# Kernel tuning notes

Measured on AMD Instinct MI355X. Metric: run time of the kernel, lower is better.

The kernel has to match this reference:

```python
import jax, jax.numpy as jnp
import numpy as np

EPS = 1e-5

def batchnorm2d(x, gamma, beta):
    # training-mode BN over (N, T, V) per channel; x: [N, C, T, V]
    mean = jnp.mean(x, axis=(0, 2, 3), keepdims=True)
    var = jnp.var(x, axis=(0, 2, 3), keepdims=True)
    xhat = (x - mean) * jax.lax.rsqrt(var + EPS)
    return xhat * gamma[None, :, None, None] + beta[None, :, None, None]

def temporal_shift(x, theta, stride):
    # learnable per-channel temporal shift with linear interpolation, zero pad
    # x: [N, C, T, V], theta: [C]
    N, C, T, V = x.shape
    T_out = T // stride
    t = jnp.arange(T_out, dtype=theta.dtype)
    pos = t[None, :] * stride + theta[:, None]          # [C, T_out]
    i0 = jnp.floor(pos).astype(jnp.int32)
    frac = (pos - i0.astype(theta.dtype))[None, :, :, None]  # [1,C,T_out,1]
    cidx = jnp.arange(C)[:, None]                        # [C, 1]

    def gather(idx):
        valid = (idx >= 0) & (idx < T)
        g = x[:, cidx, jnp.clip(idx, 0, T - 1), :]       # [N, C, T_out, V]
        return jnp.where(valid[None, :, :, None], g, 0.0)

    return gather(i0) * (1.0 - frac) + gather(i0 + 1) * frac

def setup_inputs() -> dict:
    key = jax.random.key(0)
    k = jax.random.split(key, 6)
    N, Cin, Cout, T, V = 64, 256, 256, 64, 25
    x = jax.random.normal(k[0], (N, Cin, T, V), dtype=jnp.float32)
    # kaiming normal fan_out for 1x1 conv: std = sqrt(2 / (Cout*1*1))
    conv_w = jax.random.normal(k[1], (Cout, Cin), dtype=jnp.float32) * np.float32(np.sqrt(2.0 / Cout))
    conv_b = jnp.zeros((Cout,), dtype=jnp.float32)
    bn1_g = jnp.ones((Cin,), dtype=jnp.float32)
    bn1_b = jnp.zeros((Cin,), dtype=jnp.float32)
    bn2_g = jnp.ones((Cin,), dtype=jnp.float32)   # bn_init(bn2, 1)
    bn2_b = jnp.zeros((Cin,), dtype=jnp.float32)
    theta_in = jax.random.uniform(k[2], (Cin,), jnp.float32, -1.0, 1.0)
    theta_out = jax.random.uniform(k[3], (Cout,), jnp.float32, -1.0, 1.0)
    return {"x": x, "conv_w": conv_w, "conv_b": conv_b,
            "bn1_g": bn1_g, "bn1_b": bn1_b, "bn2_g": bn2_g, "bn2_b": bn2_b,
            "theta_in": theta_in, "theta_out": theta_out}

def reference(x, conv_w, conv_b, bn1_g, bn1_b, bn2_g, bn2_b, theta_in, theta_out):
    stride = 1
    h = batchnorm2d(x, bn1_g, bn1_b)
    h = temporal_shift(h, theta_in, 1)
    h = jnp.einsum('nctv,oc->notv', h, conv_w) + conv_b[None, :, None, None]
    h = jax.nn.relu(h)
    h = temporal_shift(h, theta_out, stride)
    h = batchnorm2d(h, bn2_g, bn2_b)
    return h
```

## Files before the change

### kernel.cpp

```cpp
#include <hip/hip_runtime.h>


#define EPSV 1e-5f
constexpr int Nn = 64, Cc = 256, Tt = 64, Vv = 25;
constexpr int TV = Tt * Vv;
constexpr int CTV = Cc * TV;
constexpr float Minv = 1.0f / (Nn * TV);

typedef short short8 __attribute__((ext_vector_type(8)));
typedef float floatx4 __attribute__((ext_vector_type(4)));

__device__ __forceinline__ unsigned short f2bf(float f) {
    unsigned int u = __builtin_bit_cast(unsigned int, f);
    u += 0x7FFFu + ((u >> 16) & 1u);
    return (unsigned short)(u >> 16);
}
__device__ __forceinline__ float bf2f(unsigned short h) {
    unsigned int u = ((unsigned int)h) << 16;
    return __builtin_bit_cast(float, u);
}
__device__ __forceinline__ void gload_lds16(const void* g, void* l) {
    __builtin_amdgcn_global_load_lds((const __attribute__((address_space(1))) void*)g,
                                     (__attribute__((address_space(3))) void*)l, 16, 0, 0);
}

__global__ __launch_bounds__(256) void k_bn1_stats(const float* __restrict__ x,
                                                   const float* __restrict__ w,
                                                   unsigned short* __restrict__ wb,
                                                   float* __restrict__ sacc,
                                                   float* __restrict__ qacc) {
    int c = blockIdx.y, ng = blockIdx.x, tid = threadIdx.x;
    if (c == 256) {
        int base = ng * 8192 + tid;
#pragma unroll
        for (int i = 0; i < 32; ++i) wb[base + i * 256] = f2bf(w[base + i * 256]);
        return;
    }
    const float* xp = x + (size_t)(ng * 8) * CTV + (size_t)c * TV;
    float s = 0.f, q = 0.f;
    for (int n = 0; n < 8; ++n) {
        const float4* p = (const float4*)(xp + (size_t)n * CTV);
        for (int i = tid; i < 400; i += 256) {
            float4 v = p[i];
            s += (v.x + v.y) + (v.z + v.w);
            q += (v.x * v.x + v.y * v.y) + (v.z * v.z + v.w * v.w);
        }
    }
    for (int off = 32; off; off >>= 1) { s += __shfl_down(s, off); q += __shfl_down(q, off); }
    if ((tid & 63) == 0) { atomicAdd(&sacc[c], s); atomicAdd(&qacc[c], q); }
}

__global__ __launch_bounds__(256) void k_bn1_shift(const float* __restrict__ x,
                                                   const float* __restrict__ sacc,
                                                   const float* __restrict__ qacc,
                                                   const float* __restrict__ g,
                                                   const float* __restrict__ b,
                                                   const float* __restrict__ theta,
                                                   unsigned short* __restrict__ ht) {
    int c0 = blockIdx.x * 16;
    int tile = blockIdx.y;
    int n = blockIdx.z;
    int tid = threadIdx.x;
    __shared__ __attribute__((aligned(16))) float lds[16][460];
    __shared__ float psc[16], ptc[16], pfr[16];
    __shared__ int pdd[16], pww[16];

    if (tid < 16) {
        int c = c0 + tid;
        float mean = sacc[c] * Minv;
        float var = qacc[c] * Minv - mean * mean;
        float sc = g[c] * rsqrtf(var + EPSV);
        float th = theta[c];
        float fd = floorf(th);
        int d = (int)fd;
        pdd[tid] = d;
        pww[tid] = 28 + d * 25;
        pfr[tid] = th - fd;
        psc[tid] = sc;
        ptc[tid] = b[c] - mean * sc;
    }

    int E0 = tile * 400;
    int lo = E0 - 28; if (lo < 0) lo = 0;
    int hi = E0 + 428; if (hi > 1600) hi = 1600;
    int ldsoff = lo - (E0 - 28);
    int nf4 = (hi - lo) >> 2;
    {
        int ci = tid >> 4, li = tid & 15;
        const float4* xrow = (const float4*)(x + (size_t)n * CTV + (size_t)(c0 + ci) * TV + lo);
        float* lrow = &lds[ci][ldsoff];
        for (int i = li; i < nf4; i += 16)
            *(float4*)(lrow + i * 4) = xrow[i];
    }
    __syncthreads();

    int oct = tid & 1, tvr = tid >> 1;
    unsigned short* outb = ht + (size_t)n * CTV + c0 + oct * 8;
    for (int tv_l = tvr; tv_l < 400; tv_l += 128) {
        int e = E0 + tv_l;
        int t = e / 25;
        unsigned int wrds[4];
#pragma unroll
        for (int k = 0; k < 8; ++k) {
            int ci = oct * 8 + k;
            int i0 = t + pdd[ci];
            int w0 = tv_l + pww[ci];
            float x0 = lds[ci][w0];
            float x1 = lds[ci][w0 + 25];
            float sc = psc[ci], tc = ptc[ci], f = pfr[ci];
            float b0 = ((unsigned)i0 < 64u) ? (x0 * sc + tc) : 0.f;
            float b1 = ((unsigned)(i0 + 1) < 64u) ? (x1 * sc + tc) : 0.f;
            unsigned short hb = f2bf(b0 + f * (b1 - b0));
            if (k & 1) wrds[k >> 1] |= ((unsigned int)hb) << 16;
            else       wrds[k >> 1] = hb;
        }
        uint4 st = { wrds[0], wrds[1], wrds[2], wrds[3] };
        *(uint4*)(outb + (size_t)e * 256) = st;
    }
}

__global__ __launch_bounds__(256) void k_gemm(const unsigned short* __restrict__ ht,
                                              const unsigned short* __restrict__ wb,
                                              const float* __restrict__ bias,
                                              unsigned short* __restrict__ y) {
    int j0 = blockIdx.x * 128;
    int o0 = blockIdx.y * 128;
    int tid = threadIdx.x;
    int w = tid >> 6, lane = tid & 63;
    int quad = lane >> 4, l16 = lane & 15;
    __shared__ __attribute__((aligned(16))) unsigned short A[128 * 32];
    __shared__ __attribute__((aligned(16))) unsigned short B[128 * 32];
    floatx4 acc[4][4] = {};
    int srow = w * 32 + (lane >> 2);
    int skcol = (lane & 3) * 8;
    const unsigned short* wp0 = wb + (size_t)(o0 + srow) * 256 + skcol;
    const unsigned short* hp0 = ht + (size_t)(j0 + srow) * 256 + skcol;
    int oh = w >> 1, jh = w & 1;
    for (int k0 = 0; k0 < 256; k0 += 32) {
        __syncthreads();
#pragma unroll
        for (int a = 0; a < 2; ++a) {
            gload_lds16(wp0 + (size_t)a * 16 * 256 + k0, A + (w * 32 + a * 16) * 32);
            gload_lds16(hp0 + (size_t)a * 16 * 256 + k0, B + (w * 32 + a * 16) * 32);
        }
        __syncthreads();
        short8 af[4], bf[4];
#pragma unroll
        for (int m = 0; m < 4; ++m)
            af[m] = *(const short8*)&A[(oh * 64 + m * 16 + l16) * 32 + quad * 8];
#pragma unroll
        for (int jt = 0; jt < 4; ++jt)
            bf[jt] = *(const short8*)&B[(jh * 64 + jt * 16 + l16) * 32 + quad * 8];
#pragma unroll
        for (int m = 0; m < 4; ++m)
#pragma unroll
            for (int jt = 0; jt < 4; ++jt)
                acc[m][jt] = __builtin_amdgcn_mfma_f32_16x16x32_bf16(af[m], bf[jt], acc[m][jt], 0, 0, 0);
    }
    int jbase = j0 + jh * 64;
    int n = jbase / 1600;
    int tvb = jbase - n * 1600;
    unsigned short* yb = y + (size_t)n * CTV + tvb;
#pragma unroll
    for (int m = 0; m < 4; ++m) {
        int o = o0 + oh * 64 + m * 16 + quad * 4;
#pragma unroll
        for (int r = 0; r < 4; ++r) {
            float bia = bias[o + r];
            unsigned short* yrow = yb + (size_t)(o + r) * TV;
#pragma unroll
            for (int jt = 0; jt < 4; ++jt) {
                float vv = acc[m][jt][r] + bia;
                vv = vv > 0.f ? vv : 0.f;
                yrow[jt * 16 + l16] = f2bf(vv);
            }
        }
    }
}

__global__ __launch_bounds__(256) void k_bn2_stats(const unsigned short* __restrict__ y,
                                                   const float* __restrict__ theta,
                                                   float* __restrict__ sacc,
                                                   float* __restrict__ qacc) {
    int o = blockIdx.y, ng = blockIdx.x, tid = threadIdx.x;
    __shared__ __attribute__((aligned(16))) unsigned short row[1600];
    float th = theta[o];
    float fd = floorf(th);
    int d = (int)fd;
    float f = th - fd;
    float s = 0.f, q = 0.f;
    for (int n = ng * 8; n < ng * 8 + 8; ++n) {
        const uint4* yp = (const uint4*)(y + (size_t)n * CTV + (size_t)o * TV);
        __syncthreads();
        if (tid < 200) ((uint4*)row)[tid] = yp[tid];
        __syncthreads();
        for (int e = tid; e < 1600; e += 256) {
            int t = e / 25, v = e - t * 25;
            int i0 = t + d, i1 = i0 + 1;
            float a0 = ((unsigned)i0 < 64u) ? bf2f(row[i0 * 25 + v]) : 0.f;
            float a1 = ((unsigned)i1 < 64u) ? bf2f(row[i1 * 25 + v]) : 0.f;
            float z = (1.f - f) * a0 + f * a1;
            s += z; q += z * z;
        }
    }
    for (int off = 32; off; off >>= 1) { s += __shfl_down(s, off); q += __shfl_down(q, off); }
    if ((tid & 63) == 0) { atomicAdd(&sacc[o], s); atomicAdd(&qacc[o], q); }
}

__global__ __launch_bounds__(256) void k_bn2_apply(const unsigned short* __restrict__ y,
                                                   const float* __restrict__ theta,
                                                   const float* __restrict__ sacc,
                                                   const float* __restrict__ qacc,
                                                   const float* __restrict__ g,
                                                   const float* __restrict__ b,
                                                   float* __restrict__ out) {
    int o = blockIdx.y, n = blockIdx.x, tid = threadIdx.x;
    __shared__ __attribute__((aligned(16))) unsigned short row[1600];
    float th = theta[o];
    float fd = floorf(th);
    int d = (int)fd;
    float f = th - fd;
    float mean = sacc[o] * Minv;
    float var = qacc[o] * Minv - mean * mean;
    float sc = g[o] * rsqrtf(var + EPSV);
    float tc = b[o] - mean * sc;
    const uint4* yp = (const uint4*)(y + (size_t)n * CTV + (size_t)o * TV);
    if (tid < 200) ((uint4*)row)[tid] = yp[tid];
    __syncthreads();
    float4* op = (float4*)(out + (size_t)n * CTV + (size_t)o * TV);
    for (int i = tid; i < 400; i += 256) {
        float4 r;
        int e = i * 4;
#pragma unroll
        for (int k = 0; k < 4; ++k) {
            int ee = e + k;
            int t = ee / 25, v = ee - t * 25;
            int i0 = t + d, i1 = i0 + 1;
            float a0 = ((unsigned)i0 < 64u) ? bf2f(row[i0 * 25 + v]) : 0.f;
            float a1 = ((unsigned)i1 < 64u) ? bf2f(row[i1 * 25 + v]) : 0.f;
            ((float*)&r)[k] = ((1.f - f) * a0 + f * a1) * sc + tc;
        }
        op[i] = r;
    }
}

extern "C" void kernel_launch(void* const* d_in, const int* in_sizes, int n_in,
                              void* d_out, int out_size, void* d_ws, size_t ws_size,
                              hipStream_t stream) {
    const float* x      = (const float*)d_in[0];
    const float* conv_w = (const float*)d_in[1];
    const float* conv_b = (const float*)d_in[2];
    const float* bn1_g  = (const float*)d_in[3];
    const float* bn1_b  = (const float*)d_in[4];
    const float* bn2_g  = (const float*)d_in[5];
    const float* bn2_b  = (const float*)d_in[6];
    const float* th_in  = (const float*)d_in[7];
    const float* th_out = (const float*)d_in[8];
    float* out = (float*)d_out;

    char* ws = (char*)d_ws;
    unsigned short* ht = (unsigned short*)ws;
    unsigned short* yy = (unsigned short*)(ws + 52428800);
    unsigned short* wb = (unsigned short*)(ws + 104857600);
    float* sacc1 = (float*)(ws + 104988672);
    float* qacc1 = sacc1 + 256;
    float* sacc2 = qacc1 + 256;
    float* qacc2 = sacc2 + 256;

    hipMemsetAsync((void*)sacc1, 0, 4 * 256 * sizeof(float), stream);
    hipLaunchKernelGGL(k_bn1_stats, dim3(8, 257), dim3(256), 0, stream,
                       x, conv_w, wb, sacc1, qacc1);
    hipLaunchKernelGGL(k_bn1_shift, dim3(16, 4, 64), dim3(256), 0, stream,
                       x, sacc1, qacc1, bn1_g, bn1_b, th_in, ht);
    hipLaunchKernelGGL(k_gemm, dim3(800, 2), dim3(256), 0, stream, ht, wb, conv_b, yy);
    hipLaunchKernelGGL(k_bn2_stats, dim3(8, 256), dim3(256), 0, stream, yy, th_out, sacc2, qacc2);
    hipLaunchKernelGGL(k_bn2_apply, dim3(64, 256), dim3(256), 0, stream,
                       yy, th_out, sacc2, qacc2, bn2_g, bn2_b, out);
}
```

Baseline: 328.2 us.

## Fold BN1 affine into GEMM weights and fuse BN1 stats with temporal shift

BN1 normalization is folded algebraically into the 1x1 conv: weights are scaled by the per-channel BN scale, and the shift term becomes a per-output bias, with edge corrections at t=0 and t=63 for the zero padding. This lets one kernel read x once, computing BN1 stats and writing the shifted bf16 activations without waiting for stats, which removes a full pass over x. The GEMM tile also grows to cover all 256 outputs per block, and the output is staged through LDS so global stores are coalesced. The risks are bf16 rounding of the raw, unnormalized shifted input and of the scaled weights, the larger LDS and register footprint, and the correctness of the boundary bias corrections.

```diff
diff --git a/kernel.cpp b/kernel.cpp
--- a/kernel.cpp
+++ b/kernel.cpp
@@ -24,157 +24,199 @@
                                      (__attribute__((address_space(3))) void*)l, 16, 0, 0);
 }
 
-__global__ __launch_bounds__(256) void k_bn1_stats(const float* __restrict__ x,
-                                                   const float* __restrict__ w,
-                                                   unsigned short* __restrict__ wb,
-                                                   float* __restrict__ sacc,
-                                                   float* __restrict__ qacc) {
-    int c = blockIdx.y, ng = blockIdx.x, tid = threadIdx.x;
-    if (c == 256) {
-        int base = ng * 8192 + tid;
-#pragma unroll
-        for (int i = 0; i < 32; ++i) wb[base + i * 256] = f2bf(w[base + i * 256]);
-        return;
-    }
-    const float* xp = x + (size_t)(ng * 8) * CTV + (size_t)c * TV;
-    float s = 0.f, q = 0.f;
-    for (int n = 0; n < 8; ++n) {
-        const float4* p = (const float4*)(xp + (size_t)n * CTV);
-        for (int i = tid; i < 400; i += 256) {
-            float4 v = p[i];
-            s += (v.x + v.y) + (v.z + v.w);
-            q += (v.x * v.x + v.y * v.y) + (v.z * v.z + v.w * v.w);
-        }
-    }
-    for (int off = 32; off; off >>= 1) { s += __shfl_down(s, off); q += __shfl_down(q, off); }
-    if ((tid & 63) == 0) { atomicAdd(&sacc[c], s); atomicAdd(&qacc[c], q); }
-}
-
-__global__ __launch_bounds__(256) void k_bn1_shift(const float* __restrict__ x,
-                                                   const float* __restrict__ sacc,
-                                                   const float* __restrict__ qacc,
-                                                   const float* __restrict__ g,
-                                                   const float* __restrict__ b,
-                                                   const float* __restrict__ theta,
-                                                   unsigned short* __restrict__ ht) {
-    int c0 = blockIdx.x * 16;
-    int tile = blockIdx.y;
-    int n = blockIdx.z;
+__global__ __launch_bounds__(256) void k_stats_shift(const float* __restrict__ x,
+                                                     const float* __restrict__ theta,
+                                                     float* __restrict__ sacc,
+                                                     float* __restrict__ qacc,
+                                                     unsigned short* __restrict__ ht) {
+    int c0 = blockIdx.x * 64;
+    int E0 = blockIdx.y * 200;
+    int n  = blockIdx.z;
     int tid = threadIdx.x;
-    __shared__ __attribute__((aligned(16))) float lds[16][460];
-    __shared__ float psc[16], ptc[16], pfr[16];
-    __shared__ int pdd[16], pww[16];
-
-    if (tid < 16) {
-        int c = c0 + tid;
-        float mean = sacc[c] * Minv;
-        float var = qacc[c] * Minv - mean * mean;
-        float sc = g[c] * rsqrtf(var + EPSV);
-        float th = theta[c];
+    __shared__ __attribute__((aligned(16))) float xt[256][68];
+    __shared__ int   pd[64];
+    __shared__ float pf[64];
+    if (tid < 64) {
+        float th = theta[c0 + tid];
         float fd = floorf(th);
-        int d = (int)fd;
-        pdd[tid] = d;
-        pww[tid] = 28 + d * 25;
-        pfr[tid] = th - fd;
-        psc[tid] = sc;
-        ptc[tid] = b[c] - mean * sc;
-    }
-
-    int E0 = tile * 400;
+        pd[tid] = (int)fd;
+        pf[tid] = th - fd;
+    }
     int lo = E0 - 28; if (lo < 0) lo = 0;
-    int hi = E0 + 428; if (hi > 1600) hi = 1600;
+    int hi = E0 + 228; if (hi > 1600) hi = 1600;
     int ldsoff = lo - (E0 - 28);
     int nf4 = (hi - lo) >> 2;
     {
-        int ci = tid >> 4, li = tid & 15;
+        int ci = tid >> 2, li = tid & 3;
         const float4* xrow = (const float4*)(x + (size_t)n * CTV + (size_t)(c0 + ci) * TV + lo);
-        float* lrow = &lds[ci][ldsoff];
-        for (int i = li; i < nf4; i += 16)
-            *(float4*)(lrow + i * 4) = xrow[i];
-    }
-    __syncthreads();
-
-    int oct = tid & 1, tvr = tid >> 1;
-    unsigned short* outb = ht + (size_t)n * CTV + c0 + oct * 8;
-    for (int tv_l = tvr; tv_l < 400; tv_l += 128) {
+        for (int i = li; i < nf4; i += 4) {
+            float4 v = xrow[i];
+            int r = ldsoff + i * 4;
+            xt[r][ci] = v.x; xt[r + 1][ci] = v.y; xt[r + 2][ci] = v.z; xt[r + 3][ci] = v.w;
+        }
+    }
+    __syncthreads();
+    {
+        int ci = tid >> 2, li = tid & 3;
+        float s = 0.f, q = 0.f;
+        for (int r = 28 + li; r < 228; r += 4) {
+            float v = xt[r][ci];
+            s += v; q += v * v;
+        }
+        s += __shfl_down(s, 2); q += __shfl_down(q, 2);
+        s += __shfl_down(s, 1); q += __shfl_down(q, 1);
+        if (li == 0) { atomicAdd(&sacc[c0 + ci], s); atomicAdd(&qacc[c0 + ci], q); }
+    }
+    int cseg = tid & 7, er = tid >> 3;
+    int cb = cseg * 8;
+    for (int it = 0; it < 7; ++it) {
+        int tv_l = er + it * 32;
+        if (tv_l >= 200) break;
         int e = E0 + tv_l;
         int t = e / 25;
-        unsigned int wrds[4];
+        const float* rA = &xt[tv_l + 3][cb];
+        const float* rB = &xt[tv_l + 28][cb];
+        const float* rC = &xt[tv_l + 53][cb];
+        float4 a0 = *(const float4*)rA, a1 = *(const float4*)(rA + 4);
+        float4 b0 = *(const float4*)rB, b1 = *(const float4*)(rB + 4);
+        float4 g0 = *(const float4*)rC, g1 = *(const float4*)(rC + 4);
+        float A8[8] = {a0.x, a0.y, a0.z, a0.w, a1.x, a1.y, a1.z, a1.w};
+        float B8[8] = {b0.x, b0.y, b0.z, b0.w, b1.x, b1.y, b1.z, b1.w};
+        float C8[8] = {g0.x, g0.y, g0.z, g0.w, g1.x, g1.y, g1.z, g1.w};
+        unsigned int w4[4];
 #pragma unroll
         for (int k = 0; k < 8; ++k) {
-            int ci = oct * 8 + k;
-            int i0 = t + pdd[ci];
-            int w0 = tv_l + pww[ci];
-            float x0 = lds[ci][w0];
-            float x1 = lds[ci][w0 + 25];
-            float sc = psc[ci], tc = ptc[ci], f = pfr[ci];
-            float b0 = ((unsigned)i0 < 64u) ? (x0 * sc + tc) : 0.f;
-            float b1 = ((unsigned)(i0 + 1) < 64u) ? (x1 * sc + tc) : 0.f;
-            unsigned short hb = f2bf(b0 + f * (b1 - b0));
-            if (k & 1) wrds[k >> 1] |= ((unsigned int)hb) << 16;
-            else       wrds[k >> 1] = hb;
-        }
-        uint4 st = { wrds[0], wrds[1], wrds[2], wrds[3] };
-        *(uint4*)(outb + (size_t)e * 256) = st;
-    }
-}
-
-__global__ __launch_bounds__(256) void k_gemm(const unsigned short* __restrict__ ht,
-                                              const unsigned short* __restrict__ wb,
-                                              const float* __restrict__ bias,
-                                              unsigned short* __restrict__ y) {
+            int c = cb + k;
+            int d = pd[c]; float f = pf[c];
+            int i0 = t + d;
+            float x0 = (d < 0) ? A8[k] : B8[k];
+            float x1 = (d < 0) ? B8[k] : C8[k];
+            float v0 = ((unsigned)i0 < 64u) ? x0 : 0.f;
+            float v1 = ((unsigned)(i0 + 1) < 64u) ? x1 : 0.f;
+            unsigned short hb = f2bf(v0 + f * (v1 - v0));
+            if (k & 1) w4[k >> 1] |= ((unsigned int)hb) << 16;
+            else       w4[k >> 1] = hb;
+        }
+        uint4 st = { w4[0], w4[1], w4[2], w4[3] };
+        *(uint4*)(ht + (size_t)(n * 1600 + e) * 256 + c0 + cb) = st;
+    }
+}
+
+__global__ __launch_bounds__(256) void k_params(const float* __restrict__ w,
+                                                const float* __restrict__ bias,
+                                                const float* __restrict__ sacc,
+                                                const float* __restrict__ qacc,
+                                                const float* __restrict__ g,
+                                                const float* __restrict__ b,
+                                                const float* __restrict__ theta,
+                                                unsigned short* __restrict__ wb,
+                                                float* __restrict__ b2all,
+                                                float* __restrict__ s0v,
+                                                float* __restrict__ s63v) {
+    int o = blockIdx.x, c = threadIdx.x;
+    float mean = sacc[c] * Minv;
+    float var  = qacc[c] * Minv - mean * mean;
+    float sc = g[c] * rsqrtf(var + EPSV);
+    float tc = b[c] - mean * sc;
+    float th = theta[c];
+    float fd = floorf(th);
+    int d = (int)fd;
+    float f = th - fd;
+    float wv = w[o * 256 + c];
+    wb[o * 256 + c] = f2bf(wv * sc);
+    float wtc = wv * tc;
+    float r0  = (d < 0) ? wtc * (1.f - f) : 0.f;
+    float r63 = (d == 0) ? wtc * f : 0.f;
+    for (int off = 32; off; off >>= 1) {
+        wtc += __shfl_down(wtc, off);
+        r0  += __shfl_down(r0, off);
+        r63 += __shfl_down(r63, off);
+    }
+    __shared__ float aux[3][4];
+    if ((c & 63) == 0) { int wv_i = c >> 6; aux[0][wv_i] = wtc; aux[1][wv_i] = r0; aux[2][wv_i] = r63; }
+    __syncthreads();
+    if (c == 0) {
+        float sw  = aux[0][0] + aux[0][1] + aux[0][2] + aux[0][3];
+        float s0  = aux[1][0] + aux[1][1] + aux[1][2] + aux[1][3];
+        float s63 = aux[2][0] + aux[2][1] + aux[2][2] + aux[2][3];
+        b2all[o] = bias[o] + sw;
+        s0v[o] = s0;
+        s63v[o] = s63;
+    }
+}
+
+__global__ __launch_bounds__(256, 2) void k_gemm(const unsigned short* __restrict__ ht,
+                                                 const unsigned short* __restrict__ wb,
+                                                 const float* __restrict__ b2all,
+                                                 const float* __restrict__ s0v,
+                                                 const float* __restrict__ s63v,
+                                                 unsigned short* __restrict__ y) {
     int j0 = blockIdx.x * 128;
-    int o0 = blockIdx.y * 128;
     int tid = threadIdx.x;
     int w = tid >> 6, lane = tid & 63;
     int quad = lane >> 4, l16 = lane & 15;
-    __shared__ __attribute__((aligned(16))) unsigned short A[128 * 32];
-    __shared__ __attribute__((aligned(16))) unsigned short B[128 * 32];
-    floatx4 acc[4][4] = {};
-    int srow = w * 32 + (lane >> 2);
-    int skcol = (lane & 3) * 8;
-    const unsigned short* wp0 = wb + (size_t)(o0 + srow) * 256 + skcol;
-    const unsigned short* hp0 = ht + (size_t)(j0 + srow) * 256 + skcol;
-    int oh = w >> 1, jh = w & 1;
+    __shared__ __attribute__((aligned(16))) unsigned short smem[256 * 136];
+    unsigned short* A = smem;
+    unsigned short* B = smem + 256 * 32;
+    floatx4 acc[4][8] = {};
+    int srowA = w * 64 + (lane >> 2);
+    int srowB = w * 32 + (lane >> 2);
+    int skc = (lane & 3) * 8;
+    const unsigned short* wp = wb + (size_t)srowA * 256 + skc;
+    const unsigned short* hp = ht + (size_t)(j0 + srowB) * 256 + skc;
     for (int k0 = 0; k0 < 256; k0 += 32) {
         __syncthreads();
 #pragma unroll
-        for (int a = 0; a < 2; ++a) {
-            gload_lds16(wp0 + (size_t)a * 16 * 256 + k0, A + (w * 32 + a * 16) * 32);
-            gload_lds16(hp0 + (size_t)a * 16 * 256 + k0, B + (w * 32 + a * 16) * 32);
-        }
+        for (int a = 0; a < 4; ++a)
+            gload_lds16(wp + (size_t)a * 16 * 256 + k0, A + (w * 64 + a * 16) * 32);
+#pragma unroll
+        for (int a = 0; a < 2; ++a)
+            gload_lds16(hp + (size_t)a * 16 * 256 + k0, B + (w * 32 + a * 16) * 32);
         __syncthreads();
-        short8 af[4], bf[4];
+        short8 af[4], bf[8];
 #pragma unroll
         for (int m = 0; m < 4; ++m)
-            af[m] = *(const short8*)&A[(oh * 64 + m * 16 + l16) * 32 + quad * 8];
-#pragma unroll
-        for (int jt = 0; jt < 4; ++jt)
-            bf[jt] = *(const short8*)&B[(jh * 64 + jt * 16 + l16) * 32 + quad * 8];
+            af[m] = *(const short8*)&A[(w * 64 + m * 16 + l16) * 32 + quad * 8];
+#pragma unroll
+        for (int jt = 0; jt < 8; ++jt)
+            bf[jt] = *(const short8*)&B[(jt * 16 + l16) * 32 + quad * 8];
 #pragma unroll
         for (int m = 0; m < 4; ++m)
 #pragma unroll
-            for (int jt = 0; jt < 4; ++jt)
+            for (int jt = 0; jt < 8; ++jt)
                 acc[m][jt] = __builtin_amdgcn_mfma_f32_16x16x32_bf16(af[m], bf[jt], acc[m][jt], 0, 0, 0);
     }
-    int jbase = j0 + jh * 64;
-    int n = jbase / 1600;
-    int tvb = jbase - n * 1600;
-    unsigned short* yb = y + (size_t)n * CTV + tvb;
+    __syncthreads();
+    unsigned short* Cl = smem;
 #pragma unroll
     for (int m = 0; m < 4; ++m) {
-        int o = o0 + oh * 64 + m * 16 + quad * 4;
+        int ob = w * 64 + m * 16 + quad * 4;
 #pragma unroll
         for (int r = 0; r < 4; ++r) {
-            float bia = bias[o + r];
-            unsigned short* yrow = yb + (size_t)(o + r) * TV;
-#pragma unroll
-            for (int jt = 0; jt < 4; ++jt) {
-                float vv = acc[m][jt][r] + bia;
-                vv = vv > 0.f ? vv : 0.f;
-                yrow[jt * 16 + l16] = f2bf(vv);
+            int o = ob + r;
+            float bb = b2all[o], e0 = s0v[o], e63 = s63v[o];
+#pragma unroll
+            for (int jt = 0; jt < 8; ++jt) {
+                int jj = j0 + jt * 16;
+                int nn = jj / 1600;
+                int tvb = jj - nn * 1600 + l16;
+                float bia = bb - (tvb < 25 ? e0 : 0.f) - (tvb >= 1575 ? e63 : 0.f);
+                float v = acc[m][jt][r] + bia;
+                v = v > 0.f ? v : 0.f;
+                Cl[o * 136 + jt * 16 + l16] = f2bf(v);
             }
         }
+    }
+    __syncthreads();
+    int li = tid & 15, orow = tid >> 4;
+#pragma unroll
+    for (int pass = 0; pass < 16; ++pass) {
+        int o = orow + pass * 16;
+        uint4 vv = *(const uint4*)&Cl[o * 136 + li * 8];
+        int j = j0 + li * 8;
+        int nn = j / 1600;
+        int tv = j - nn * 1600;
+        *(uint4*)(y + (size_t)nn * CTV + (size_t)o * TV + tv) = vv;
     }
 }
 
@@ -266,13 +308,18 @@
     float* qacc1 = sacc1 + 256;
     float* sacc2 = qacc1 + 256;
     float* qacc2 = sacc2 + 256;
+    float* b2all = qacc2 + 256;
+    float* s0v   = b2all + 256;
+    float* s63v  = s0v + 256;
 
     hipMemsetAsync((void*)sacc1, 0, 4 * 256 * sizeof(float), stream);
-    hipLaunchKernelGGL(k_bn1_stats, dim3(8, 257), dim3(256), 0, stream,
-                       x, conv_w, wb, sacc1, qacc1);
-    hipLaunchKernelGGL(k_bn1_shift, dim3(16, 4, 64), dim3(256), 0, stream,
-                       x, sacc1, qacc1, bn1_g, bn1_b, th_in, ht);
-    hipLaunchKernelGGL(k_gemm, dim3(800, 2), dim3(256), 0, stream, ht, wb, conv_b, yy);
+    hipLaunchKernelGGL(k_stats_shift, dim3(4, 8, 64), dim3(256), 0, stream,
+                       x, th_in, sacc1, qacc1, ht);
+    hipLaunchKernelGGL(k_params, dim3(256), dim3(256), 0, stream,
+                       conv_w, conv_b, sacc1, qacc1, bn1_g, bn1_b, th_in,
+                       wb, b2all, s0v, s63v);
+    hipLaunchKernelGGL(k_gemm, dim3(800), dim3(256), 0, stream,
+                       ht, wb, b2all, s0v, s63v, yy);
     hipLaunchKernelGGL(k_bn2_stats, dim3(8, 256), dim3(256), 0, stream, yy, th_out, sacc2, qacc2);
     hipLaunchKernelGGL(k_bn2_apply, dim3(64, 256), dim3(256), 0, stream,
                        yy, th_out, sacc2, qacc2, bn2_g, bn2_b, out);
```

New measurement: 315.7 us. -3.8%, faster.
